# Kernel optimization log

Hardware: AMD Instinct MI355X
Metric: run time of the kernel (lower is better)

The kernel has to match this reference:

```python
import jax, jax.numpy as jnp
import numpy as np

VOCAB = 128
EMB = 16
HID = 512
B, T = 128, 1024


def setup_inputs() -> dict:
    key = jax.random.key(0)
    ks = jax.random.split(key, 8)
    s = 0.05
    return {
        "x": jax.random.randint(ks[0], (B, T), 0, VOCAB),
        "emb": jax.random.normal(ks[1], (VOCAB, EMB), jnp.float32) * s,
        "W_ih": jax.random.normal(ks[2], (HID, EMB), jnp.float32) * s,
        "W_hh": jax.random.normal(ks[3], (HID, HID), jnp.float32) * s,
        "b_ih": jax.random.normal(ks[4], (HID,), jnp.float32) * s,
        "b_hh": jax.random.normal(ks[5], (HID,), jnp.float32) * s,
        "W_fc": jax.random.normal(ks[6], (VOCAB, HID), jnp.float32) * s,
        "b_fc": jax.random.normal(ks[7], (VOCAB,), jnp.float32) * s,
    }


def reference(x, emb, W_ih, W_hh, b_ih, b_hh, W_fc, b_fc):
    # Embedding lookup: [B, T, EMB]
    xe = emb[x]
    # Precompute input-to-hidden part for all steps: [B, T, HID]
    xp = jnp.einsum('bte,he->bth', xe, W_ih) + b_ih + b_hh
    h0 = jnp.zeros((xe.shape[0], W_hh.shape[0]), xe.dtype)

    def step(h, xt):  # xt: [B, HID]
        h_new = jnp.tanh(xt + h @ W_hh.T)
        return h_new, h_new

    # scan over time: [T, B, HID]
    _, hs = jax.lax.scan(step, h0, jnp.swapaxes(xp, 0, 1))
    hs = jnp.swapaxes(hs, 0, 1)  # [B, T, HID]
    logits = jnp.einsum('bth,vh->btv', hs, W_fc) + b_fc  # [B, T, VOCAB]
    return logits
```

## Files before the change

kernel.cpp:

```cpp
#include <hip/hip_runtime.h>
#include <cstdint>


typedef short bf16x8 __attribute__((ext_vector_type(8)));
typedef float f32x4 __attribute__((ext_vector_type(4)));

#define VOCAB 128
#define EMB   16
#define HID   512
#define TT    1024
#define NCL   8
#define BB    16
#define JC    32
#define NWG   128
#define BUFW  (NCL * BB * HID)
#define CNTOFF (2 * BUFW)
#define PJC   33

__device__ __forceinline__ unsigned short f2bf(float f) {
  uint32_t u = __builtin_bit_cast(uint32_t, f);
  u += 0x7FFFu + ((u >> 16) & 1u);
  return (unsigned short)(u >> 16);
}
__device__ __forceinline__ float bf2f(unsigned short s) {
  uint32_t u = (uint32_t)s << 16;
  return __builtin_bit_cast(float, u);
}
__device__ __forceinline__ float ftanh(float z) {
  z = fminf(15.f, fmaxf(-15.f, z));
  float e = __expf(2.f * z);
  return (e - 1.f) * __builtin_amdgcn_rcpf(e + 1.f);
}
__device__ __forceinline__ uint32_t aload(const uint32_t* p) {
  return __hip_atomic_load(p, __ATOMIC_RELAXED, __HIP_MEMORY_SCOPE_AGENT);
}
__device__ __forceinline__ void astore(uint32_t* p, uint32_t v) {
  __hip_atomic_store(p, v, __ATOMIC_RELAXED, __HIP_MEMORY_SCOPE_AGENT);
}

__global__ __launch_bounds__(256, 1) void charrnn_kernel(
    const int* __restrict__ xin,
    const float* __restrict__ emb,
    const float* __restrict__ wih,
    const float* __restrict__ whh,
    const float* __restrict__ bih,
    const float* __restrict__ bhh,
    const float* __restrict__ wfc,
    const float* __restrict__ bfc,
    float* __restrict__ out,
    uint32_t* __restrict__ hx)
{
  __shared__ __align__(16) unsigned short a_hi[16 * 512];
  __shared__ __align__(16) unsigned short a_lo[16 * 512];
  __shared__ float ep[VOCAB * PJC];
  __shared__ unsigned char xtok[BB * TT];
  __shared__ __align__(16) float red[2][256];

  const int tid  = threadIdx.x;
  const int wave = tid >> 6;
  const int lane = tid & 63;
  const int col  = lane & 15;
  const int quad = lane >> 4;
  const int cl   = blockIdx.x & 7;
  const int m    = blockIdx.x >> 3;

  bf16x8 wfh[16], wfl[16], wfcf[8];
  if (wave < 2) {
    const int nrow = m * JC + wave * 16 + col;
    const float* wr = whh + (size_t)nrow * HID + quad * 8;
    #pragma unroll
    for (int ks = 0; ks < 16; ++ks) {
      bf16x8 hi, lo;
      #pragma unroll
      for (int j = 0; j < 8; ++j) {
        float w = wr[ks * 32 + j];
        unsigned short h = f2bf(w);
        hi[j] = (short)h;
        lo[j] = (short)f2bf(w - bf2f(h));
      }
      wfh[ks] = hi; wfl[ks] = lo;
    }
  } else {
    const int vrow = m * 8 + (col & 7);
    const float* wr = wfc + (size_t)vrow * HID + (wave - 2) * 256 + quad * 8;
    #pragma unroll
    for (int ks = 0; ks < 8; ++ks) {
      bf16x8 f;
      #pragma unroll
      for (int j = 0; j < 8; ++j) f[j] = (short)f2bf(wr[ks * 32 + j]);
      wfcf[ks] = f;
    }
  }
  const float bfcr = bfc[m * 8 + (col & 7)];

  for (int i = tid; i < 16 * 512; i += 256) { a_hi[i] = 0; a_lo[i] = 0; }
  for (int i = tid; i < VOCAB * JC; i += 256) {
    int v = i >> 5, jl = i & 31;
    int jg = m * JC + jl;
    float s = bih[jg] + bhh[jg];
    #pragma unroll
    for (int e = 0; e < EMB; ++e) s += emb[v * EMB + e] * wih[jg * EMB + e];
    ep[v * PJC + jl] = s;
  }
  for (int i = tid; i < BB * TT; i += 256) {
    int b = i >> 10, t = i & 1023;
    xtok[i] = (unsigned char)xin[(cl * BB + b) * TT + t];
  }
  __syncthreads();

  const int lw = tid & 31;
  const int r0 = tid >> 5;
  const float rcp20 = 1.f / 1048576.f;
  uint32_t* const cnt = hx + CNTOFF + cl * 32;
  f32x4 prev_lacc = {0.f, 0.f, 0.f, 0.f};

  #pragma unroll 1
  for (int t = 0; t <= TT + 1; ++t) {
    const int par = t & 1;
    const uint32_t tag = (uint32_t)t & 0x7FFu;
    uint32_t* const p0 = hx + par * BUFW + (cl * BB + r0) * HID + lw;
    uint32_t* const p1 = p0 + 8 * HID;

    if (wave >= 2 && t >= 2) {
      *(f32x4*)&red[wave - 2][lane * 4] = prev_lacc;
    }

    if (t >= 1 && t <= TT) {
      const uint32_t target = 32u * (uint32_t)t;
      while ((int32_t)(aload(cnt) - target) < 0) {}

      const int qk = lw >> 3, jj = lw & 7;
      const int idx0 = ((qk << 4) + r0) * 8 + jj;
      const int idx1 = idx0 + 64;
      for (;;) {
        uint32_t v0[16], v1[16];
        #pragma unroll
        for (int i = 0; i < 16; ++i) v0[i] = aload(p0 + 32 * i);
        #pragma unroll
        for (int i = 0; i < 16; ++i) v1[i] = aload(p1 + 32 * i);
        uint32_t bad = 0;
        #pragma unroll
        for (int i = 0; i < 16; ++i) bad |= (v0[i] ^ tag) | (v1[i] ^ tag);
        if ((bad & 0x7FFu) == 0) {
          #pragma unroll
          for (int i = 0; i < 16; ++i) {
            float h0 = (float)(((int)v0[i]) >> 11) * rcp20;
            uint32_t uh0 = __builtin_bit_cast(uint32_t, h0) & 0xFFFF0000u;
            float l0 = h0 - __builtin_bit_cast(float, uh0);
            a_hi[i * 512 + idx0] = (unsigned short)(uh0 >> 16);
            a_lo[i * 512 + idx0] = (unsigned short)(__builtin_bit_cast(uint32_t, l0) >> 16);
            float h1 = (float)(((int)v1[i]) >> 11) * rcp20;
            uint32_t uh1 = __builtin_bit_cast(uint32_t, h1) & 0xFFFF0000u;
            float l1 = h1 - __builtin_bit_cast(float, uh1);
            a_hi[i * 512 + idx1] = (unsigned short)(uh1 >> 16);
            a_lo[i * 512 + idx1] = (unsigned short)(__builtin_bit_cast(uint32_t, l1) >> 16);
          }
          break;
        }
      }
    }
    __syncthreads();

    if (wave < 2) {
      if (t < TT) {
        f32x4 acc0 = {0.f,0.f,0.f,0.f}, acc1 = {0.f,0.f,0.f,0.f}, acc2 = {0.f,0.f,0.f,0.f};
        #pragma unroll
        for (int ks = 0; ks < 16; ++ks) {
          bf16x8 ah = *(const bf16x8*)&a_hi[ks * 512 + lane * 8];
          bf16x8 al = *(const bf16x8*)&a_lo[ks * 512 + lane * 8];
          acc0 = __builtin_amdgcn_mfma_f32_16x16x32_bf16(ah, wfh[ks], acc0, 0, 0, 0);
          acc1 = __builtin_amdgcn_mfma_f32_16x16x32_bf16(al, wfh[ks], acc1, 0, 0, 0);
          acc2 = __builtin_amdgcn_mfma_f32_16x16x32_bf16(ah, wfl[ks], acc2, 0, 0, 0);
        }
        const int jl = wave * 16 + col;
        const uint32_t ntag = (uint32_t)(t + 1) & 0x7FFu;
        uint32_t* wb = hx + ((t + 1) & 1) * BUFW + (cl * BB) * HID + m * JC + jl;
        #pragma unroll
        for (int i = 0; i < 4; ++i) {
          const int b = quad * 4 + i;
          float z = acc0[i] + acc1[i] + acc2[i]
                  + ep[(int)xtok[b * TT + t] * PJC + jl];
          float h = ftanh(z);
          int q = __float2int_rn(h * 1048576.f);
          q = max(min(q, 1048575), -1048576);
          astore(wb + b * HID, ((uint32_t)q << 11) | ntag);
        }
        if (lane == 0)
          (void)__hip_atomic_fetch_add(cnt, 1u, __ATOMIC_RELAXED,
                                       __HIP_MEMORY_SCOPE_AGENT);
      }
    } else {
      if (wave == 2 && t >= 2 && col < 8) {
        #pragma unroll
        for (int i = 0; i < 4; ++i) {
          const int b = quad * 4 + i;
          float s = red[0][lane * 4 + i] + red[1][lane * 4 + i] + bfcr;
          out[((size_t)(cl * BB + b) * TT + (t - 2)) * VOCAB + m * 8 + col] = s;
        }
      }
      if (t >= 1 && t <= TT) {
        f32x4 lacc = {0.f, 0.f, 0.f, 0.f};
        const int kb = (wave - 2) * 8;
        #pragma unroll
        for (int ks = 0; ks < 8; ++ks) {
          bf16x8 ah = *(const bf16x8*)&a_hi[(kb + ks) * 512 + lane * 8];
          bf16x8 al = *(const bf16x8*)&a_lo[(kb + ks) * 512 + lane * 8];
          lacc = __builtin_amdgcn_mfma_f32_16x16x32_bf16(ah, wfcf[ks], lacc, 0, 0, 0);
          lacc = __builtin_amdgcn_mfma_f32_16x16x32_bf16(al, wfcf[ks], lacc, 0, 0, 0);
        }
        prev_lacc = lacc;
      }
    }
    __syncthreads();
  }
}

extern "C" void kernel_launch(void* const* d_in, const int* in_sizes, int n_in,
                              void* d_out, int out_size, void* d_ws, size_t ws_size,
                              hipStream_t stream) {
  (void)in_sizes; (void)n_in; (void)out_size;
  if (ws_size < (size_t)CNTOFF * sizeof(uint32_t) + 4096) return;

  const int*   x    = (const int*)d_in[0];
  const float* embp = (const float*)d_in[1];
  const float* W_ih = (const float*)d_in[2];
  const float* W_hh = (const float*)d_in[3];
  const float* b_ih = (const float*)d_in[4];
  const float* b_hh = (const float*)d_in[5];
  const float* W_fc = (const float*)d_in[6];
  const float* b_fc = (const float*)d_in[7];

  hipMemsetAsync((uint32_t*)d_ws + CNTOFF, 0, NCL * 32 * sizeof(uint32_t), stream);

  charrnn_kernel<<<NWG, 256, 0, stream>>>(x, embp, W_ih, W_hh, b_ih, b_hh, W_fc, b_fc,
                                          (float*)d_out, (uint32_t*)d_ws);
}
```

Before: 3.285 ms.

## Exchange hidden state as pre-split bf16 hi/lo in MFMA layout with per-wave flags

Producers now split h into bf16 hi and lo halves themselves, pair them across lanes with a shuffle, and store them directly in the LDS operand layout. Consumers can then copy the data with plain 32-bit loads and no conversion. The old scheme (20-bit fixed-point words tagged with a step number, a shared atomic counter, and tag-validation retries) is replaced by per-wave step flags written after an s_waitcnt and polled with a wave-wide __all. The goal is to shorten the per-step critical path between workgroups. The trade-off is that correctness now relies on the flag store becoming visible after the data stores, using only relaxed atomics plus vmcnt.

```diff
diff --git a/kernel.cpp b/kernel.cpp
--- a/kernel.cpp
+++ b/kernel.cpp
@@ -13,8 +13,9 @@
 #define BB    16
 #define JC    32
 #define NWG   128
-#define BUFW  (NCL * BB * HID)
-#define CNTOFF (2 * BUFW)
+#define CLW   8192
+#define BUFW  (NCL * CLW)
+#define FLAGOFF (2 * BUFW)
 #define PJC   33
 
 __device__ __forceinline__ unsigned short f2bf(float f) {
@@ -108,56 +109,34 @@
   }
   __syncthreads();
 
-  const int lw = tid & 31;
-  const int r0 = tid >> 5;
-  const float rcp20 = 1.f / 1048576.f;
-  uint32_t* const cnt = hx + CNTOFF + cl * 32;
+  uint32_t* const flags = hx + FLAGOFF + cl * 32;
   f32x4 prev_lacc = {0.f, 0.f, 0.f, 0.f};
 
   #pragma unroll 1
   for (int t = 0; t <= TT + 1; ++t) {
     const int par = t & 1;
-    const uint32_t tag = (uint32_t)t & 0x7FFu;
-    uint32_t* const p0 = hx + par * BUFW + (cl * BB + r0) * HID + lw;
-    uint32_t* const p1 = p0 + 8 * HID;
 
     if (wave >= 2 && t >= 2) {
       *(f32x4*)&red[wave - 2][lane * 4] = prev_lacc;
     }
 
     if (t >= 1 && t <= TT) {
-      const uint32_t target = 32u * (uint32_t)t;
-      while ((int32_t)(aload(cnt) - target) < 0) {}
-
-      const int qk = lw >> 3, jj = lw & 7;
-      const int idx0 = ((qk << 4) + r0) * 8 + jj;
-      const int idx1 = idx0 + 64;
-      for (;;) {
-        uint32_t v0[16], v1[16];
-        #pragma unroll
-        for (int i = 0; i < 16; ++i) v0[i] = aload(p0 + 32 * i);
-        #pragma unroll
-        for (int i = 0; i < 16; ++i) v1[i] = aload(p1 + 32 * i);
-        uint32_t bad = 0;
-        #pragma unroll
-        for (int i = 0; i < 16; ++i) bad |= (v0[i] ^ tag) | (v1[i] ^ tag);
-        if ((bad & 0x7FFu) == 0) {
-          #pragma unroll
-          for (int i = 0; i < 16; ++i) {
-            float h0 = (float)(((int)v0[i]) >> 11) * rcp20;
-            uint32_t uh0 = __builtin_bit_cast(uint32_t, h0) & 0xFFFF0000u;
-            float l0 = h0 - __builtin_bit_cast(float, uh0);
-            a_hi[i * 512 + idx0] = (unsigned short)(uh0 >> 16);
-            a_lo[i * 512 + idx0] = (unsigned short)(__builtin_bit_cast(uint32_t, l0) >> 16);
-            float h1 = (float)(((int)v1[i]) >> 11) * rcp20;
-            uint32_t uh1 = __builtin_bit_cast(uint32_t, h1) & 0xFFFF0000u;
-            float l1 = h1 - __builtin_bit_cast(float, uh1);
-            a_hi[i * 512 + idx1] = (unsigned short)(uh1 >> 16);
-            a_lo[i * 512 + idx1] = (unsigned short)(__builtin_bit_cast(uint32_t, l1) >> 16);
-          }
-          break;
-        }
-      }
+      uint32_t f;
+      do {
+        f = aload(&flags[lane & 31]);
+      } while (__all((int)(f >= (uint32_t)t)) == 0);
+      asm volatile("" ::: "memory");
+
+      const uint32_t* src = hx + par * BUFW + cl * CLW + tid;
+      uint32_t v[32];
+      #pragma unroll
+      for (int i = 0; i < 32; ++i) v[i] = aload(src + 256 * i);
+      #pragma unroll
+      for (int i = 0; i < 16; ++i)
+        *(uint32_t*)&a_hi[(tid + 256 * i) * 2] = v[i];
+      #pragma unroll
+      for (int i = 0; i < 16; ++i)
+        *(uint32_t*)&a_lo[(tid + 256 * i) * 2] = v[16 + i];
     }
     __syncthreads();
 
@@ -173,21 +152,26 @@
           acc2 = __builtin_amdgcn_mfma_f32_16x16x32_bf16(ah, wfl[ks], acc2, 0, 0, 0);
         }
         const int jl = wave * 16 + col;
-        const uint32_t ntag = (uint32_t)(t + 1) & 0x7FFu;
-        uint32_t* wb = hx + ((t + 1) & 1) * BUFW + (cl * BB) * HID + m * JC + jl;
+        uint32_t* wb = hx + ((t + 1) & 1) * BUFW + cl * CLW
+                     + ((lane & 1) ? 4096 : 0)
+                     + m * 256 + (wave * 2 + (col >> 3)) * 64 + ((col & 7) >> 1);
         #pragma unroll
         for (int i = 0; i < 4; ++i) {
           const int b = quad * 4 + i;
           float z = acc0[i] + acc1[i] + acc2[i]
                   + ep[(int)xtok[b * TT + t] * PJC + jl];
           float h = ftanh(z);
-          int q = __float2int_rn(h * 1048576.f);
-          q = max(min(q, 1048575), -1048576);
-          astore(wb + b * HID, ((uint32_t)q << 11) | ntag);
-        }
-        if (lane == 0)
-          (void)__hip_atomic_fetch_add(cnt, 1u, __ATOMIC_RELAXED,
-                                       __HIP_MEMORY_SCOPE_AGENT);
+          unsigned short hi = f2bf(h);
+          float lof = h - bf2f(hi);
+          unsigned short lo = f2bf(lof);
+          uint32_t pk = (uint32_t)hi | ((uint32_t)lo << 16);
+          uint32_t pp = (uint32_t)__shfl_xor((int)pk, 1);
+          uint32_t word = (lane & 1) ? ((pp >> 16) | (pk & 0xFFFF0000u))
+                                     : ((pk & 0xFFFFu) | (pp << 16));
+          astore(wb + b * 4, word);
+        }
+        asm volatile("s_waitcnt vmcnt(0)" ::: "memory");
+        if (lane == 0) astore(&flags[m * 2 + wave], (uint32_t)(t + 1));
       }
     } else {
       if (wave == 2 && t >= 2 && col < 8) {
@@ -219,7 +203,7 @@
                               void* d_out, int out_size, void* d_ws, size_t ws_size,
                               hipStream_t stream) {
   (void)in_sizes; (void)n_in; (void)out_size;
-  if (ws_size < (size_t)CNTOFF * sizeof(uint32_t) + 4096) return;
+  if (ws_size < (size_t)FLAGOFF * sizeof(uint32_t) + 4096) return;
 
   const int*   x    = (const int*)d_in[0];
   const float* embp = (const float*)d_in[1];
@@ -230,7 +214,7 @@
   const float* W_fc = (const float*)d_in[6];
   const float* b_fc = (const float*)d_in[7];
 
-  hipMemsetAsync((uint32_t*)d_ws + CNTOFF, 0, NCL * 32 * sizeof(uint32_t), stream);
+  hipMemsetAsync((uint32_t*)d_ws + FLAGOFF, 0, NCL * 32 * sizeof(uint32_t), stream);
 
   charrnn_kernel<<<NWG, 256, 0, stream>>>(x, embp, W_ih, W_hh, b_ih, b_hh, W_fc, b_fc,
                                           (float*)d_out, (uint32_t*)d_ws);
```

Result: faster. 3.018 ms (-8.1%).
